# Performance work log

Measured on AMD Instinct MI355X. Metric: run time of the kernel, lower is better.

## Reference

```python
import math
import jax, jax.numpy as jnp
import numpy as np

VMIN, VMAX = 0.0, 1.0
NUM_BINS = 64
SIGMA = 0.5 * (VMAX - VMIN) / NUM_BINS  # matches torch: sigma * (vmax-vmin)/num_bins
EPS = 1e-10


def setup_inputs() -> dict:
    key = jax.random.key(0)
    k1, k2 = jax.random.split(key)
    shape = (2, 1, 96, 96, 96)
    tar = jax.random.uniform(k1, shape, dtype=jnp.float32)
    src = jax.random.uniform(k2, shape, dtype=jnp.float32)
    return {"tar": tar, "src": src}


def _normalise_minmax(x, min_out, max_out):
    # x: (N, P) -- per-sample min-max normalisation to [min_out, max_out]
    xmin = jnp.min(x, axis=1, keepdims=True)
    xmax = jnp.max(x, axis=1, keepdims=True)
    return (x - xmin) / (xmax - xmin + EPS) * (max_out - min_out) + min_out


def _windowed(x, bins):
    # x: (N, P), bins: (B,) -> (N, B, P) Gaussian kernel weights
    d = x[:, None, :] - bins[None, :, None]
    return jnp.exp(-(d * d) / (2.0 * SIGMA * SIGMA)) / math.sqrt(2.0 * math.pi) * SIGMA


def reference(tar, src):
    N = tar.shape[0]
    # use channel 0 only, flatten spatial dims
    t = _normalise_minmax(tar[:, 0].reshape(N, -1), VMIN, VMAX)
    s = _normalise_minmax(src[:, 0].reshape(N, -1), VMIN, VMAX)

    bins = jnp.linspace(VMIN, VMAX, NUM_BINS, dtype=tar.dtype)
    w_tar = _windowed(t, bins)  # (N, B, P)
    w_src = _windowed(s, bins)  # (N, B, P)

    hist_joint = jnp.einsum('nbp,ncp->nbc', w_tar, w_src)  # (N, B, B)
    hist_norm = jnp.sum(hist_joint, axis=(1, 2), keepdims=True)
    p_joint = hist_joint / hist_norm

    p_tar = jnp.sum(p_joint, axis=2)  # (N, B)
    p_src = jnp.sum(p_joint, axis=1)  # (N, B)

    ent_tar = -jnp.sum(p_tar * jnp.log(p_tar + EPS), axis=1)
    ent_src = -jnp.sum(p_src * jnp.log(p_src + EPS), axis=1)
    ent_joint = -jnp.sum(p_joint * jnp.log(p_joint + EPS), axis=(1, 2))

    # normalised=True branch
    return -jnp.mean((ent_tar + ent_src) / ent_joint)
```

## Files before the change

kernel.cpp:

```cpp
#include <hip/hip_runtime.h>
#include <math.h>

#define NBINS 64
#define HIST_ELEMS (NBINS*NBINS)
#define PTS_PER_BLOCK 3456
#define GXN 256
#define CHUNKS 27
#define LSTRIDE 68
#define SQK 1.7256062f
#define SMEM_FLOATS (2*PTS_PER_BLOCK + NBINS*LSTRIDE)

typedef float f4 __attribute__((ext_vector_type(4)));
typedef float f32x4 __attribute__((ext_vector_type(4)));
typedef _Float16 half8 __attribute__((ext_vector_type(8)));
typedef int int4v __attribute__((ext_vector_type(4)));

static __device__ __forceinline__ half8 pack8(const float* w) {
    int4v v;
    v[0] = __builtin_bit_cast(int, __builtin_amdgcn_cvt_pkrtz(w[0], w[1]));
    v[1] = __builtin_bit_cast(int, __builtin_amdgcn_cvt_pkrtz(w[2], w[3]));
    v[2] = __builtin_bit_cast(int, __builtin_amdgcn_cvt_pkrtz(w[4], w[5]));
    v[3] = __builtin_bit_cast(int, __builtin_amdgcn_cvt_pkrtz(w[6], w[7]));
    return __builtin_bit_cast(half8, v);
}

__global__ __launch_bounds__(256) void minmax_kernel(const float* __restrict__ tar,
                                                     const float* __restrict__ src,
                                                     float* __restrict__ pm,
                                                     unsigned* __restrict__ ctr,
                                                     float* __restrict__ hist, int P) {
    const int b = blockIdx.x, n = blockIdx.y, t = blockIdx.z;
    const f4* x = (const f4*)((t == 0 ? tar : src) + (size_t)n * P);
    const int per = (P / 4) / 64;
    float lmin = INFINITY, lmax = -INFINITY;
    for (int i = b * per + threadIdx.x; i < (b + 1) * per; i += 256) {
        f4 v = x[i];
        lmin = fminf(lmin, fminf(fminf(v[0], v[1]), fminf(v[2], v[3])));
        lmax = fmaxf(lmax, fmaxf(fmaxf(v[0], v[1]), fmaxf(v[2], v[3])));
    }
    for (int off = 32; off > 0; off >>= 1) {
        lmin = fminf(lmin, __shfl_down(lmin, off, 64));
        lmax = fmaxf(lmax, __shfl_down(lmax, off, 64));
    }
    __shared__ float smin[4], smax[4];
    const int lane = threadIdx.x & 63, wave = threadIdx.x >> 6;
    if (lane == 0) { smin[wave] = lmin; smax[wave] = lmax; }
    __syncthreads();
    if (threadIdx.x == 0) {
        pm[(n * 2 + t) * 64 + b] =
            fminf(fminf(smin[0], smin[1]), fminf(smin[2], smin[3]));
        pm[256 + (n * 2 + t) * 64 + b] =
            fmaxf(fmaxf(smax[0], smax[1]), fmaxf(smax[2], smax[3]));
    }
    const int flat = b + 64 * n + 128 * t;
    f4* hz = (f4*)hist + flat * 8;
    const f4 z = {0.f, 0.f, 0.f, 0.f};
    if (threadIdx.x < 8) hz[threadIdx.x] = z;
    if (flat == 0 && threadIdx.x == 0) *ctr = 0u;
}

template <int STAGED>
__global__ __launch_bounds__(256) void mfma_hist_kernel(const float* __restrict__ tar,
                                                        const float* __restrict__ src,
                                                        const float* __restrict__ pm,
                                                        float* __restrict__ bh,
                                                        float* __restrict__ hist,
                                                        int P) {
    const int n = blockIdx.y;
    const int bx = blockIdx.x;
    const int tid = threadIdx.x;
    const int lane = tid & 63, wave = tid >> 6;
    const int mlane = lane & 15, quad = lane >> 4;

    __shared__ float smem[SMEM_FLOATS];
    __shared__ float mmred[4];
    float* su_t = smem;
    float* su_s = smem + PTS_PER_BLOCK;
    float* lh = smem + 2 * PTS_PER_BLOCK;

    if (wave == 0) {
        float a = pm[(n * 2 + 0) * 64 + lane];
        float b = pm[256 + (n * 2 + 0) * 64 + lane];
        float c = pm[(n * 2 + 1) * 64 + lane];
        float d = pm[256 + (n * 2 + 1) * 64 + lane];
        for (int off = 32; off > 0; off >>= 1) {
            a = fminf(a, __shfl_down(a, off, 64));
            b = fmaxf(b, __shfl_down(b, off, 64));
            c = fminf(c, __shfl_down(c, off, 64));
            d = fmaxf(d, __shfl_down(d, off, 64));
        }
        if (lane == 0) { mmred[0] = a; mmred[1] = b; mmred[2] = c; mmred[3] = d; }
    }

    {
        const f4* tg = (const f4*)(tar + (size_t)n * P + (size_t)bx * PTS_PER_BLOCK);
        const f4* sg = (const f4*)(src + (size_t)n * P + (size_t)bx * PTS_PER_BLOCK);
        f4* st4 = (f4*)su_t;
        f4* ss4 = (f4*)su_s;
        #pragma unroll
        for (int k = 0; k < 3; ++k) {
            const int i = tid + k * 256;
            st4[i] = tg[i];
            ss4[i] = sg[i];
        }
        if (tid < 96) {
            const int i = 768 + tid;
            st4[i] = tg[i];
            ss4[i] = sg[i];
        }
    }
    __syncthreads();

    const float tmin = mmred[0], tmax = mmred[1];
    const float smin = mmred[2], smax = mmred[3];
    const float tk = 63.0f / (tmax - tmin + 1e-10f) * SQK;
    const float sk = 63.0f / (smax - smin + 1e-10f) * SQK;
    float mt2[4], ms2[4];
    #pragma unroll
    for (int mt = 0; mt < 4; ++mt) {
        const float b = SQK * (float)(mlane + 16 * mt);
        mt2[mt] = tmin * tk + b;
        ms2[mt] = smin * sk + b;
    }

    f32x4 acc[4][4];
    #pragma unroll
    for (int a = 0; a < 4; ++a)
        #pragma unroll
        for (int b = 0; b < 4; ++b) acc[a][b] = (f32x4){0.f, 0.f, 0.f, 0.f};

    const int kwbase = wave * (32 * CHUNKS) + quad * 8;
    #pragma unroll 3
    for (int c = 0; c < CHUNKS; ++c) {
        const int kbase = kwbase + c * 32;
        const f4* pt4 = (const f4*)&su_t[kbase];
        const f4* ps4 = (const f4*)&su_s[kbase];
        f4 ta = pt4[0], tb = pt4[1];
        f4 sa = ps4[0], sb = ps4[1];
        float xt[8] = {ta[0], ta[1], ta[2], ta[3], tb[0], tb[1], tb[2], tb[3]};
        float xs[8] = {sa[0], sa[1], sa[2], sa[3], sb[0], sb[1], sb[2], sb[3]};

        half8 af[4], bf[4];
        #pragma unroll
        for (int mt = 0; mt < 4; ++mt) {
            float w[8];
            #pragma unroll
            for (int j = 0; j < 8; ++j) {
                float d = fmaf(xt[j], tk, -mt2[mt]);
                w[j] = __builtin_amdgcn_exp2f(-(d * d));
            }
            af[mt] = pack8(w);
        }
        #pragma unroll
        for (int nt = 0; nt < 4; ++nt) {
            float w[8];
            #pragma unroll
            for (int j = 0; j < 8; ++j) {
                float d = fmaf(xs[j], sk, -ms2[nt]);
                w[j] = __builtin_amdgcn_exp2f(-(d * d));
            }
            bf[nt] = pack8(w);
        }
        #pragma unroll
        for (int mt = 0; mt < 4; ++mt)
            #pragma unroll
            for (int nt = 0; nt < 4; ++nt)
                acc[mt][nt] = __builtin_amdgcn_mfma_f32_16x16x32_f16(
                    af[mt], bf[nt], acc[mt][nt], 0, 0, 0);
    }

    #pragma unroll
    for (int w = 0; w < 4; ++w) {
        if (wave == w) {
            #pragma unroll
            for (int nt = 0; nt < 4; ++nt)
                #pragma unroll
                for (int mt = 0; mt < 4; ++mt) {
                    f4* p = (f4*)&lh[(16 * nt + mlane) * LSTRIDE + 16 * mt + 4 * quad];
                    if (w == 0) {
                        *p = acc[mt][nt];
                    } else {
                        f4 v = *p;
                        v += acc[mt][nt];
                        *p = v;
                    }
                }
        }
        __syncthreads();
    }

    if (STAGED) {
        f4* dst = (f4*)(bh + ((size_t)n * GXN + bx) * HIST_ELEMS);
        #pragma unroll
        for (int k = 0; k < 4; ++k) {
            const int i4 = tid + k * 256;
            const int c = i4 >> 4, r4 = (i4 & 15) * 4;
            dst[i4] = *(const f4*)&lh[c * LSTRIDE + r4];
        }
    } else {
        float* gh = hist + (size_t)n * HIST_ELEMS;
        for (int i = tid; i < HIST_ELEMS; i += 256) {
            const int c = i >> 6, r = i & 63;
            unsafeAtomicAdd(&gh[i], lh[c * LSTRIDE + r]);
        }
    }
}

__global__ __launch_bounds__(256) void reduce_finalize_kernel(const float* __restrict__ bh,
                                                              float* __restrict__ hist,
                                                              unsigned* __restrict__ ctr,
                                                              float* __restrict__ out,
                                                              int staged) {
    const int tid = threadIdx.x;
    const int lane = tid & 63, wave = tid >> 6;
    __shared__ float h2[2 * HIST_ELEMS];
    __shared__ float buf[4], rowsum[NBINS], colsum[NBINS], colp[4 * NBINS];
    __shared__ int lastflag;

    if (staged) {
        const int g = blockIdx.x * 256 + tid;
        const int n = g >> 12, e = g & 4095;
        const float* p = bh + (((size_t)n * GXN) << 12) + e;
        float sum = 0.0f;
        #pragma unroll 8
        for (int b = 0; b < GXN; ++b) sum += p[(size_t)b << 12];
        hist[g] = sum;
    }

    __threadfence();
    if (tid == 0) {
        unsigned old = atomicAdd(ctr, 1u);
        lastflag = (old == 31) ? 1 : 0;
    }
    __syncthreads();
    if (!lastflag) return;

    for (int i = tid; i < 2 * HIST_ELEMS; i += 256)
        h2[i] = __hip_atomic_load(&hist[i], __ATOMIC_RELAXED, __HIP_MEMORY_SCOPE_SYSTEM);
    __syncthreads();

    float accl = 0.0f;
    for (int nn = 0; nn < 2; ++nn) {
        const float* h = h2 + nn * HIST_ELEMS;
        {
            int r = tid >> 2, q = tid & 3;
            const float* hp = h + r * NBINS + q * 16;
            float sv = 0.0f;
            #pragma unroll
            for (int k = 0; k < 16; ++k) sv += hp[k];
            sv += __shfl_down(sv, 1, 64);
            sv += __shfl_down(sv, 2, 64);
            if (q == 0) rowsum[r] = sv;
        }
        {
            int c = tid & 63, g = tid >> 6;
            const float* hp = h + (g * 16) * NBINS + c;
            float sv = 0.0f;
            #pragma unroll
            for (int k = 0; k < 16; ++k) sv += hp[k * NBINS];
            colp[g * NBINS + c] = sv;
        }
        __syncthreads();
        if (tid < NBINS)
            colsum[tid] = colp[0 * NBINS + tid] + colp[1 * NBINS + tid] +
                          colp[2 * NBINS + tid] + colp[3 * NBINS + tid];
        __syncthreads();

        float tv = (tid < NBINS) ? rowsum[tid] : 0.0f;
        for (int off = 32; off > 0; off >>= 1) tv += __shfl_down(tv, off, 64);
        __syncthreads();
        if (lane == 0) buf[wave] = tv;
        __syncthreads();
        const float total = buf[0] + buf[1] + buf[2] + buf[3];
        const float inv = 1.0f / total;

        float ej = 0.0f;
        for (int i = tid; i < HIST_ELEMS; i += 256) {
            float p = h[i] * inv;
            ej += p * __logf(p + 1e-10f);
        }
        for (int off = 32; off > 0; off >>= 1) ej += __shfl_down(ej, off, 64);
        __syncthreads();
        if (lane == 0) buf[wave] = ej;
        __syncthreads();
        const float entj = -(buf[0] + buf[1] + buf[2] + buf[3]);

        float em = 0.0f;
        if (tid < NBINS) {
            float p = rowsum[tid] * inv;
            em = p * __logf(p + 1e-10f);
        } else if (tid < 2 * NBINS) {
            float p = colsum[tid - NBINS] * inv;
            em = p * __logf(p + 1e-10f);
        }
        for (int off = 32; off > 0; off >>= 1) em += __shfl_down(em, off, 64);
        __syncthreads();
        if (lane == 0) buf[wave] = em;
        __syncthreads();
        const float ents = -(buf[0] + buf[1] + buf[2] + buf[3]);

        accl += ents / entj;
        __syncthreads();
    }
    if (tid == 0) out[0] = -0.5f * accl;
}

extern "C" void kernel_launch(void* const* d_in, const int* in_sizes, int n_in,
                              void* d_out, int out_size, void* d_ws, size_t ws_size,
                              hipStream_t stream) {
    const float* tar = (const float*)d_in[0];
    const float* src = (const float*)d_in[1];
    const int N = 2;
    const int P = in_sizes[0] / N;

    float* pm = (float*)d_ws;
    unsigned* ctr = (unsigned*)((char*)d_ws + 2048);
    float* hist = (float*)((char*)d_ws + 4096);
    float* bh = (float*)((char*)d_ws + 36864);
    float* out = (float*)d_out;

    const size_t need = 36864 + (size_t)2 * GXN * HIST_ELEMS * 4;

    minmax_kernel<<<dim3(64, N, 2), 256, 0, stream>>>(tar, src, pm, ctr, hist, P);
    if (ws_size >= need) {
        mfma_hist_kernel<1><<<dim3(GXN, N), 256, 0, stream>>>(tar, src, pm, bh, hist, P);
        reduce_finalize_kernel<<<32, 256, 0, stream>>>(bh, hist, ctr, out, 1);
    } else {
        mfma_hist_kernel<0><<<dim3(GXN, N), 256, 0, stream>>>(tar, src, pm, bh, hist, P);
        reduce_finalize_kernel<<<32, 256, 0, stream>>>(bh, hist, ctr, out, 0);
    }
}
```

Before: 133.6 us.

## Store partial histograms in fp16, retile grid, pack weight math, widen reduction

```diff
diff --git a/kernel.cpp b/kernel.cpp
--- a/kernel.cpp
+++ b/kernel.cpp
@@ -3,17 +3,21 @@
 
 #define NBINS 64
 #define HIST_ELEMS (NBINS*NBINS)
-#define PTS_PER_BLOCK 3456
-#define GXN 256
-#define CHUNKS 27
+#define PTS_PER_BLOCK 2304
+#define GXN 384
+#define CHUNKS 18
 #define LSTRIDE 68
 #define SQK 1.7256062f
 #define SMEM_FLOATS (2*PTS_PER_BLOCK + NBINS*LSTRIDE)
+#define RED_BLOCKS 128
+#define TILES_PER_WAVE (GXN/4)
 
 typedef float f4 __attribute__((ext_vector_type(4)));
+typedef float f2 __attribute__((ext_vector_type(2)));
 typedef float f32x4 __attribute__((ext_vector_type(4)));
 typedef _Float16 half8 __attribute__((ext_vector_type(8)));
 typedef int int4v __attribute__((ext_vector_type(4)));
+typedef unsigned int u32x2 __attribute__((ext_vector_type(2)));
 
 static __device__ __forceinline__ half8 pack8(const float* w) {
     int4v v;
@@ -22,6 +26,17 @@
     v[2] = __builtin_bit_cast(int, __builtin_amdgcn_cvt_pkrtz(w[4], w[5]));
     v[3] = __builtin_bit_cast(int, __builtin_amdgcn_cvt_pkrtz(w[6], w[7]));
     return __builtin_bit_cast(half8, v);
+}
+
+static __device__ __forceinline__ f2 pk_fma(f2 a, f2 b, f2 c) {
+    f2 d;
+    asm("v_pk_fma_f32 %0, %1, %2, %3" : "=v"(d) : "v"(a), "v"(b), "v"(c));
+    return d;
+}
+static __device__ __forceinline__ f2 pk_mul(f2 a, f2 b) {
+    f2 d;
+    asm("v_pk_mul_f32 %0, %1, %2" : "=v"(d) : "v"(a), "v"(b));
+    return d;
 }
 
 __global__ __launch_bounds__(256) void minmax_kernel(const float* __restrict__ tar,
@@ -63,7 +78,7 @@
 __global__ __launch_bounds__(256) void mfma_hist_kernel(const float* __restrict__ tar,
                                                         const float* __restrict__ src,
                                                         const float* __restrict__ pm,
-                                                        float* __restrict__ bh,
+                                                        _Float16* __restrict__ bh,
                                                         float* __restrict__ hist,
                                                         int P) {
     const int n = blockIdx.y;
@@ -98,13 +113,13 @@
         f4* st4 = (f4*)su_t;
         f4* ss4 = (f4*)su_s;
         #pragma unroll
-        for (int k = 0; k < 3; ++k) {
+        for (int k = 0; k < 2; ++k) {
             const int i = tid + k * 256;
             st4[i] = tg[i];
             ss4[i] = sg[i];
         }
-        if (tid < 96) {
-            const int i = 768 + tid;
+        if (tid < 64) {
+            const int i = 512 + tid;
             st4[i] = tg[i];
             ss4[i] = sg[i];
         }
@@ -115,12 +130,15 @@
     const float smin = mmred[2], smax = mmred[3];
     const float tk = 63.0f / (tmax - tmin + 1e-10f) * SQK;
     const float sk = 63.0f / (smax - smin + 1e-10f) * SQK;
-    float mt2[4], ms2[4];
+    const f2 tkk = {tk, tk}, skk = {sk, sk};
+    f2 tneg[4], sneg[4];
     #pragma unroll
     for (int mt = 0; mt < 4; ++mt) {
         const float b = SQK * (float)(mlane + 16 * mt);
-        mt2[mt] = tmin * tk + b;
-        ms2[mt] = smin * sk + b;
+        const float tb_ = tmin * tk + b;
+        const float sb_ = smin * sk + b;
+        tneg[mt] = {-tb_, -tb_};
+        sneg[mt] = {-sb_, -sb_};
     }
 
     f32x4 acc[4][4];
@@ -137,17 +155,22 @@
         const f4* ps4 = (const f4*)&su_s[kbase];
         f4 ta = pt4[0], tb = pt4[1];
         f4 sa = ps4[0], sb = ps4[1];
-        float xt[8] = {ta[0], ta[1], ta[2], ta[3], tb[0], tb[1], tb[2], tb[3]};
-        float xs[8] = {sa[0], sa[1], sa[2], sa[3], sb[0], sb[1], sb[2], sb[3]};
+        f2 tp[4], sp[4];
+        tp[0] = {ta[0], ta[1]}; tp[1] = {ta[2], ta[3]};
+        tp[2] = {tb[0], tb[1]}; tp[3] = {tb[2], tb[3]};
+        sp[0] = {sa[0], sa[1]}; sp[1] = {sa[2], sa[3]};
+        sp[2] = {sb[0], sb[1]}; sp[3] = {sb[2], sb[3]};
 
         half8 af[4], bf[4];
         #pragma unroll
         for (int mt = 0; mt < 4; ++mt) {
             float w[8];
             #pragma unroll
-            for (int j = 0; j < 8; ++j) {
-                float d = fmaf(xt[j], tk, -mt2[mt]);
-                w[j] = __builtin_amdgcn_exp2f(-(d * d));
+            for (int h = 0; h < 4; ++h) {
+                f2 d = pk_fma(tp[h], tkk, tneg[mt]);
+                f2 s2 = pk_mul(d, d);
+                w[2 * h]     = __builtin_amdgcn_exp2f(-s2[0]);
+                w[2 * h + 1] = __builtin_amdgcn_exp2f(-s2[1]);
             }
             af[mt] = pack8(w);
         }
@@ -155,9 +178,11 @@
         for (int nt = 0; nt < 4; ++nt) {
             float w[8];
             #pragma unroll
-            for (int j = 0; j < 8; ++j) {
-                float d = fmaf(xs[j], sk, -ms2[nt]);
-                w[j] = __builtin_amdgcn_exp2f(-(d * d));
+            for (int h = 0; h < 4; ++h) {
+                f2 d = pk_fma(sp[h], skk, sneg[nt]);
+                f2 s2 = pk_mul(d, d);
+                w[2 * h]     = __builtin_amdgcn_exp2f(-s2[0]);
+                w[2 * h + 1] = __builtin_amdgcn_exp2f(-s2[1]);
             }
             bf[nt] = pack8(w);
         }
@@ -190,12 +215,16 @@
     }
 
     if (STAGED) {
-        f4* dst = (f4*)(bh + ((size_t)n * GXN + bx) * HIST_ELEMS);
+        u32x2* dst = (u32x2*)(bh + ((size_t)n * GXN + bx) * HIST_ELEMS);
         #pragma unroll
         for (int k = 0; k < 4; ++k) {
             const int i4 = tid + k * 256;
             const int c = i4 >> 4, r4 = (i4 & 15) * 4;
-            dst[i4] = *(const f4*)&lh[c * LSTRIDE + r4];
+            f4 v = *(const f4*)&lh[c * LSTRIDE + r4];
+            u32x2 o;
+            o[0] = __builtin_bit_cast(unsigned int, __builtin_amdgcn_cvt_pkrtz(v[0], v[1]));
+            o[1] = __builtin_bit_cast(unsigned int, __builtin_amdgcn_cvt_pkrtz(v[2], v[3]));
+            dst[i4] = o;
         }
     } else {
         float* gh = hist + (size_t)n * HIST_ELEMS;
@@ -206,7 +235,7 @@
     }
 }
 
-__global__ __launch_bounds__(256) void reduce_finalize_kernel(const float* __restrict__ bh,
+__global__ __launch_bounds__(256) void reduce_finalize_kernel(const _Float16* __restrict__ bh,
                                                               float* __restrict__ hist,
                                                               unsigned* __restrict__ ctr,
                                                               float* __restrict__ out,
@@ -215,22 +244,26 @@
     const int lane = tid & 63, wave = tid >> 6;
     __shared__ float h2[2 * HIST_ELEMS];
     __shared__ float buf[4], rowsum[NBINS], colsum[NBINS], colp[4 * NBINS];
+    __shared__ float part[4][64];
     __shared__ int lastflag;
 
     if (staged) {
-        const int g = blockIdx.x * 256 + tid;
+        const int g = blockIdx.x * 64 + lane;
         const int n = g >> 12, e = g & 4095;
-        const float* p = bh + (((size_t)n * GXN) << 12) + e;
-        float sum = 0.0f;
+        const _Float16* p = bh + (((size_t)(n * GXN + wave * TILES_PER_WAVE)) << 12) + e;
+        float s = 0.0f;
         #pragma unroll 8
-        for (int b = 0; b < GXN; ++b) sum += p[(size_t)b << 12];
-        hist[g] = sum;
+        for (int b = 0; b < TILES_PER_WAVE; ++b) s += (float)p[(size_t)b << 12];
+        part[wave][lane] = s;
+        __syncthreads();
+        if (wave == 0)
+            hist[g] = part[0][lane] + part[1][lane] + part[2][lane] + part[3][lane];
     }
 
     __threadfence();
     if (tid == 0) {
         unsigned old = atomicAdd(ctr, 1u);
-        lastflag = (old == 31) ? 1 : 0;
+        lastflag = (old == RED_BLOCKS - 1) ? 1 : 0;
     }
     __syncthreads();
     if (!lastflag) return;
@@ -316,17 +349,17 @@
     float* pm = (float*)d_ws;
     unsigned* ctr = (unsigned*)((char*)d_ws + 2048);
     float* hist = (float*)((char*)d_ws + 4096);
-    float* bh = (float*)((char*)d_ws + 36864);
+    _Float16* bh = (_Float16*)((char*)d_ws + 36864);
     float* out = (float*)d_out;
 
-    const size_t need = 36864 + (size_t)2 * GXN * HIST_ELEMS * 4;
+    const size_t need = 36864 + (size_t)2 * GXN * HIST_ELEMS * sizeof(_Float16);
 
     minmax_kernel<<<dim3(64, N, 2), 256, 0, stream>>>(tar, src, pm, ctr, hist, P);
     if (ws_size >= need) {
         mfma_hist_kernel<1><<<dim3(GXN, N), 256, 0, stream>>>(tar, src, pm, bh, hist, P);
-        reduce_finalize_kernel<<<32, 256, 0, stream>>>(bh, hist, ctr, out, 1);
+        reduce_finalize_kernel<<<RED_BLOCKS, 256, 0, stream>>>(bh, hist, ctr, out, 1);
     } else {
         mfma_hist_kernel<0><<<dim3(GXN, N), 256, 0, stream>>>(tar, src, pm, bh, hist, P);
-        reduce_finalize_kernel<<<32, 256, 0, stream>>>(bh, hist, ctr, out, 0);
-    }
-}
+        reduce_finalize_kernel<<<RED_BLOCKS, 256, 0, stream>>>(bh, hist, ctr, out, 0);
+    }
+}
```

After: 129.2 us. 3.3% less time.
